# Kernel tuning notes

Hardware: AMD Instinct MI355X
Metric: run time of the kernel (lower is better)

Reference implementation:

```python
import jax, jax.numpy as jnp
import numpy as np

IMAGE_TOKEN = 32000
PAD_TOKEN = 0
IGNORE_INDEX = -100
PATCH = 14
B, S = 8, 1024
IMG = 336
VOCAB = 32064
D = 4096          # text embed_dim
DV = 1024         # vision hidden
N_LAYERS, N_EXPERTS, N_SHARED = 32, 8, 2
NP = (IMG // PATCH) ** 2          # 576 patches after dropping CLS
MAXE = (NP - 1) + S               # one <image> token per row -> 1599


def setup_inputs() -> dict:
    key = jax.random.key(0)
    ks = jax.random.split(key, 12)
    input_ids = jax.random.randint(ks[0], (B, S), 1, IMAGE_TOKEN)  # avoid pad(0) and image token
    input_ids = input_ids.at[:, 5].set(IMAGE_TOKEN)                # exactly one image token per row
    pixel_values = jax.random.normal(ks[1], (B, 3, IMG, IMG), jnp.float32)
    attention_mask = jnp.ones((B, S), jnp.int32)
    labels = jax.random.randint(ks[2], (B, S), 0, IMAGE_TOKEN)
    embed_table = jax.random.normal(ks[3], (VOCAB, D), jnp.float32) * 0.02
    cls_emb = jax.random.normal(ks[4], (DV,), jnp.float32) * 0.02
    patch_w = jax.random.normal(ks[5], (3 * PATCH * PATCH, DV), jnp.float32) * 0.02
    patch_b = jax.random.normal(ks[6], (DV,), jnp.float32) * 0.02
    proj_w1 = jax.random.normal(ks[7], (DV, D), jnp.float32) * 0.02
    proj_b1 = jax.random.normal(ks[8], (D,), jnp.float32) * 0.02
    proj_w2 = jax.random.normal(ks[9], (D, D), jnp.float32) * 0.02
    proj_b2 = jax.random.normal(ks[10], (D,), jnp.float32) * 0.02
    return dict(input_ids=input_ids, pixel_values=pixel_values, attention_mask=attention_mask,
                labels=labels, embed_table=embed_table, cls_emb=cls_emb, patch_w=patch_w,
                patch_b=patch_b, proj_w1=proj_w1, proj_b1=proj_b1, proj_w2=proj_w2, proj_b2=proj_b2)


def _vision_project(pixel_values, cls_emb, patch_w, patch_b, w1, b1, w2, b2):
    # Vision tower stub: patchify + linear patch embedding, CLS prepended,
    # then 'default' select strategy drops CLS, then 2-layer GELU projector.
    n = pixel_values.shape[0]
    g = IMG // PATCH
    x = pixel_values.reshape(n, 3, g, PATCH, g, PATCH)
    x = x.transpose(0, 2, 4, 1, 3, 5).reshape(n, g * g, 3 * PATCH * PATCH)
    h = x @ patch_w + patch_b                                   # [n, 576, DV]
    hidden = jnp.concatenate([jnp.broadcast_to(cls_emb, (n, 1, DV)), h], axis=1)  # [n, 577, DV]
    sel = hidden[:, 1:]                                          # drop CLS ('default')
    return jax.nn.gelu(sel @ w1 + b1) @ w2 + b2                  # [n, 576, D]


def _merge(image_features, inputs_embeds, input_ids, attention_mask, labels):
    b, s = input_ids.shape
    n, p, d = image_features.shape
    special = input_ids == IMAGE_TOKEN                           # [B,S]
    left_padding = jnp.sum(input_ids[:, -1] == PAD_TOKEN) == 0
    new_pos = jnp.cumsum(special.astype(jnp.int32) * (p - 1) + 1, axis=-1) - 1
    nb_pad = MAXE - 1 - new_pos[:, -1]
    new_pos = new_pos + jnp.where(left_padding, nb_pad[:, None], 0)
    pos_safe = jnp.where(special, MAXE, new_pos)                 # OOB index for image tokens -> dropped
    bi = jnp.arange(b)[:, None]
    final_emb = jnp.zeros((b, MAXE, d), inputs_embeds.dtype).at[bi, pos_safe].set(inputs_embeds, mode='drop')
    final_attn = jnp.zeros((b, MAXE), attention_mask.dtype).at[bi, pos_safe].set(attention_mask, mode='drop')
    final_labels = jnp.full((b, MAXE), IGNORE_INDEX, labels.dtype).at[bi, pos_safe].set(labels, mode='drop')
    img_ow = jnp.all(final_emb == 0, axis=-1)                    # slots never written by text
    img_ow = img_ow & (jnp.cumsum(img_ow.astype(jnp.int32), axis=-1) - 1 >= nb_pad[:, None])
    flat_mask = img_ow.reshape(-1)                               # [B*MAXE]
    rank = jnp.cumsum(flat_mask.astype(jnp.int32)) - 1           # row-major rank of each True slot
    img_flat = image_features.reshape(-1, d)                     # [n*p, D]
    gathered = img_flat[jnp.clip(rank, 0, img_flat.shape[0] - 1)]
    final_emb = jnp.where(flat_mask[:, None], gathered, final_emb.reshape(-1, d)).reshape(b, MAXE, d)
    final_attn = jnp.where(img_ow, jnp.ones_like(final_attn), final_attn)
    return final_emb, final_attn, final_labels


def reference(input_ids, pixel_values, attention_mask, labels, embed_table, cls_emb,
              patch_w, patch_b, proj_w1, proj_b1, proj_w2, proj_b2):
    inputs_embeds = embed_table[input_ids]                       # [B,S,D]
    image_features = _vision_project(pixel_values, cls_emb, patch_w, patch_b,
                                     proj_w1, proj_b1, proj_w2, proj_b2)
    final_emb, final_attn, final_labels = _merge(image_features, inputs_embeds,
                                                 input_ids, attention_mask, labels)
    # torch.empty buffers (uninitialized scratch) -> zeros for determinism
    router_logits = jnp.zeros((N_LAYERS, MAXE, N_EXPERTS), jnp.float32)
    shared_router_logits = jnp.zeros((N_LAYERS, MAXE, N_SHARED), jnp.float32)
    current_layer = jnp.int32(0)
    return (current_layer, final_emb, final_attn, final_labels, router_logits, shared_router_logits)
```

## Files before the change

kernel.cpp:

```cpp
#include <hip/hip_runtime.h>
#include <math.h>

#define B_ 8
#define S_ 1024
#define D_ 4096
#define DV_ 1024
#define NP_ 576
#define MAXE_ 1599
#define PK_ 588
#define IMG_ 336
#define GRID_ 24
#define PATCH_ 14
#define IMAGE_TOKEN_ 32000
#define PAD_TOKEN_ 0
#define NLAYERS_ 32
#define NEXP_ 8
#define NSH_ 2

#define EMB_ELEMS ((size_t)B_ * MAXE_ * D_)
#define OFF_EMB   ((size_t)1)
#define OFF_ATTN  (OFF_EMB + EMB_ELEMS)
#define OFF_LAB   (OFF_ATTN + (size_t)B_ * MAXE_)
#define OFF_ROUTER (OFF_LAB + (size_t)B_ * MAXE_)
#define ROUTER_ELEMS ((size_t)NLAYERS_ * MAXE_ * (NEXP_ + NSH_))

typedef __bf16 bf16x8 __attribute__((ext_vector_type(8)));
typedef float  f32x4  __attribute__((ext_vector_type(4)));
typedef unsigned short ushort_t;

__device__ __forceinline__ unsigned short f2bf(float f) {
    unsigned u = __float_as_uint(f);
    u += 0x7fffu + ((u >> 16) & 1u);
    return (unsigned short)(u >> 16);
}

__device__ __forceinline__ void async_copy16(const void* g, void* l) {
    __builtin_amdgcn_global_load_lds(
        (const __attribute__((address_space(1))) void*)g,
        (__attribute__((address_space(3))) void*)l, 16, 0, 0);
}

__global__ void fill_tail_kernel(float* __restrict__ out) {
    size_t i = (size_t)blockIdx.x * blockDim.x + threadIdx.x;
    if (i == 0) out[0] = 0.0f;
    for (size_t j = i; j < ROUTER_ELEMS; j += (size_t)gridDim.x * blockDim.x)
        out[OFF_ROUTER + j] = 0.0f;
}

__global__ __launch_bounds__(512) void merge_kernel(
    const int* __restrict__ input_ids, const int* __restrict__ attn_mask,
    const int* __restrict__ labels, float* __restrict__ out,
    int* __restrict__ src_index, int* __restrict__ img_pos)
{
    __shared__ int sh_nbpad[B_];
    __shared__ int sh_shift[B_];
    __shared__ int sh_nqual[B_];
    __shared__ int sh_leftpad;
    float* out_attn = out + OFF_ATTN;
    float* out_lab  = out + OFF_LAB;
    const int tid = threadIdx.x;

    for (int i = tid; i < B_ * MAXE_; i += blockDim.x) {
        src_index[i] = -1;
        out_attn[i] = 0.0f;
        out_lab[i] = -100.0f;
    }
    for (int i = tid; i < B_ * NP_; i += blockDim.x) img_pos[i] = -1;
    if (tid == 0) {
        int anypad = 0;
        for (int b = 0; b < B_; b++)
            if (input_ids[b * S_ + S_ - 1] == PAD_TOKEN_) anypad = 1;
        sh_leftpad = !anypad;
    }
    __syncthreads();

    const int wave = tid >> 6;
    const int lane = tid & 63;
    const unsigned long long below = (1ull << lane) - 1ull;

    if (wave < B_) {
        const int b = wave;
        int nspec = 0;
        for (int c = 0; c < S_; c += 64) {
            int id = input_ids[b * S_ + c + lane];
            nspec += __popcll(__ballot(id == IMAGE_TOKEN_));
        }
        int nb_pad = MAXE_ - S_ - (NP_ - 1) * nspec;
        int shift = sh_leftpad ? nb_pad : 0;
        int nholes = MAXE_ - (S_ - nspec);
        int nq = nholes - nb_pad; if (nq < 0) nq = 0;
        if (lane == 0) { sh_nbpad[b] = nb_pad; sh_shift[b] = shift; sh_nqual[b] = nq; }
        int carry = 0;
        for (int c = 0; c < S_; c += 64) {
            int t = c + lane;
            int id = input_ids[b * S_ + t];
            int spec = (id == IMAGE_TOKEN_);
            unsigned long long m = __ballot(spec);
            int nbefore = carry + __popcll(m & below);
            if (!spec) {
                int pos = t + (NP_ - 1) * nbefore + shift;
                if (pos >= 0 && pos < MAXE_) {
                    src_index[b * MAXE_ + pos] = t;
                    out_attn[b * MAXE_ + pos] = (float)attn_mask[b * S_ + t];
                    out_lab[b * MAXE_ + pos]  = (float)labels[b * S_ + t];
                }
            }
            carry += __popcll(m);
        }
    }
    __syncthreads();

    if (wave < B_) {
        const int b = wave;
        int offs = 0;
        for (int r = 0; r < b; r++) offs += sh_nqual[r];
        const int nb_pad = sh_nbpad[b];
        int hcarry = 0;
        for (int c = 0; c < MAXE_; c += 64) {
            int p = c + lane;
            int flag = 0;
            if (p < MAXE_) flag = (src_index[b * MAXE_ + p] == -1);
            unsigned long long m = __ballot(flag);
            int h = hcarry + __popcll(m & below);
            if (flag && h >= nb_pad) {
                int g = offs + (h - nb_pad);
                if (g > B_ * NP_ - 1) g = B_ * NP_ - 1;
                if (g < 0) g = 0;
                img_pos[g] = b * MAXE_ + p;
                src_index[b * MAXE_ + p] = -2;
                out_attn[b * MAXE_ + p] = 1.0f;
            }
            hcarry += __popcll(m);
        }
    }
}

__global__ void patchify_kernel(const float* __restrict__ pix, float* __restrict__ x) {
    int i = blockIdx.x * blockDim.x + threadIdx.x;
    const int total = B_ * NP_ * PK_;
    if (i >= total) return;
    int q = i % PK_;
    int t = (i / PK_) % NP_;
    int n = i / (PK_ * NP_);
    int c = q / (PATCH_ * PATCH_);
    int r = q % (PATCH_ * PATCH_);
    int py = r / PATCH_, px = r % PATCH_;
    int gy = t / GRID_, gx = t % GRID_;
    x[i] = pix[(((size_t)n * 3 + c) * IMG_ + gy * PATCH_ + py) * IMG_ + gx * PATCH_ + px];
}

__global__ __launch_bounds__(256) void transpose_bf16_kernel(
    const float* __restrict__ src, ushort_t* __restrict__ dst, int R, int C)
{
    __shared__ float tile[32][33];
    int c0 = blockIdx.x * 32, r0 = blockIdx.y * 32;
    int tx = threadIdx.x & 31, ty = threadIdx.x >> 5;
    for (int i = ty; i < 32; i += 8)
        tile[i][tx] = src[(size_t)(r0 + i) * C + c0 + tx];
    __syncthreads();
    for (int i = ty; i < 32; i += 8)
        dst[(size_t)(c0 + i) * R + r0 + tx] = f2bf(tile[tx][i]);
}

__global__ __launch_bounds__(256) void sgemm_kernel(
    const float* __restrict__ A, const float* __restrict__ Bm,
    const float* __restrict__ bias, float* __restrict__ C, ushort_t* __restrict__ Cb,
    int M, int N, int K, int mode)
{
    __shared__ float As[8][128 + 4];
    __shared__ float Bs[8][128 + 4];
    const int tid = threadIdx.x;
    const int tx = tid & 15;
    const int ty = tid >> 4;
    const int row0 = blockIdx.y * 128;
    const int col0 = blockIdx.x * 128;
    float acc[8][8];
#pragma unroll
    for (int i = 0; i < 8; i++)
#pragma unroll
        for (int j = 0; j < 8; j++) acc[i][j] = 0.0f;

    const int ar = tid >> 1;
    const int ak = (tid & 1) * 4;
    const int bk = tid >> 5;
    const int bn = (tid & 31) * 4;

    for (int k0 = 0; k0 < K; k0 += 8) {
        float4 av = make_float4(0.f, 0.f, 0.f, 0.f);
        {
            int r = row0 + ar;
            int kb = k0 + ak;
            if (r < M) {
                if (kb + 4 <= K) {
                    av = *(const float4*)(A + (size_t)r * K + kb);
                } else {
                    float tmp[4] = {0.f, 0.f, 0.f, 0.f};
                    for (int u = 0; u < 4; u++)
                        if (kb + u < K) tmp[u] = A[(size_t)r * K + kb + u];
                    av = make_float4(tmp[0], tmp[1], tmp[2], tmp[3]);
                }
            }
        }
        As[ak + 0][ar] = av.x; As[ak + 1][ar] = av.y;
        As[ak + 2][ar] = av.z; As[ak + 3][ar] = av.w;

        float4 bv = make_float4(0.f, 0.f, 0.f, 0.f);
        {
            int kr = k0 + bk;
            if (kr < K) bv = *(const float4*)(Bm + (size_t)kr * N + col0 + bn);
        }
        *(float4*)&Bs[bk][bn] = bv;
        __syncthreads();

#pragma unroll
        for (int kk = 0; kk < 8; kk++) {
            float am[8], bb[8];
#pragma unroll
            for (int i = 0; i < 8; i++) am[i] = As[kk][ty * 8 + i];
#pragma unroll
            for (int j = 0; j < 8; j++) bb[j] = Bs[kk][tx * 8 + j];
#pragma unroll
            for (int i = 0; i < 8; i++)
#pragma unroll
                for (int j = 0; j < 8; j++)
                    acc[i][j] = fmaf(am[i], bb[j], acc[i][j]);
        }
        __syncthreads();
    }

#pragma unroll
    for (int i = 0; i < 8; i++) {
        int r = row0 + ty * 8 + i;
        if (r >= M) continue;
        int c0 = col0 + tx * 8;
        float v[8];
#pragma unroll
        for (int j = 0; j < 8; j++) v[j] = acc[i][j] + bias[c0 + j];
        if (mode == 3) {
            ushort_t* dst = Cb + (size_t)r * N + c0;
#pragma unroll
            for (int j = 0; j < 8; j++) dst[j] = f2bf(v[j]);
        } else {
            float* dst = C + (size_t)r * N + c0;
            *(float4*)dst = make_float4(v[0], v[1], v[2], v[3]);
            *(float4*)(dst + 4) = make_float4(v[4], v[5], v[6], v[7]);
        }
    }
}

__global__ __launch_bounds__(256) void mfma_gemm_bt(
    const ushort_t* __restrict__ A, const ushort_t* __restrict__ Bt,
    const float* __restrict__ bias, ushort_t* __restrict__ outb,
    float* __restrict__ outf, const int* __restrict__ pos_map,
    int M, int N, int K, int mode)
{
    __shared__ ushort_t As[128 * 32];
    __shared__ ushort_t Bs[128 * 32];
    const int tid  = threadIdx.x;
    const int wave = tid >> 6;
    const int lane = tid & 63;
    const int l16  = lane & 15;
    const int quad = lane >> 4;
    const int wrow = (wave >> 1) * 64;
    const int wcol = (wave & 1) * 64;
    const int row0 = blockIdx.y * 128;
    const int col0 = blockIdx.x * 128;

    f32x4 acc[4][4];
#pragma unroll
    for (int i = 0; i < 4; i++)
#pragma unroll
        for (int j = 0; j < 4; j++) acc[i][j] = (f32x4)(0.0f);

    const int R0a = wave * 32;
    const int lr  = lane >> 2;
    const int lc  = (lane & 3) * 8;

    for (int k0 = 0; k0 < K; k0 += 32) {
#pragma unroll
        for (int i = 0; i < 2; i++) {
            int R0 = R0a + i * 16;
            const ushort_t* ga = A  + (size_t)(row0 + R0 + lr) * K + k0 + lc;
            const ushort_t* gb = Bt + (size_t)(col0 + R0 + lr) * K + k0 + lc;
            async_copy16(ga, &As[R0 * 32]);
            async_copy16(gb, &Bs[R0 * 32]);
        }
        __syncthreads();

        bf16x8 af[4], bf[4];
#pragma unroll
        for (int mt = 0; mt < 4; mt++)
            af[mt] = *(const bf16x8*)&As[(wrow + mt * 16 + l16) * 32 + quad * 8];
#pragma unroll
        for (int nt = 0; nt < 4; nt++)
            bf[nt] = *(const bf16x8*)&Bs[(wcol + nt * 16 + l16) * 32 + quad * 8];
#pragma unroll
        for (int mt = 0; mt < 4; mt++)
#pragma unroll
            for (int nt = 0; nt < 4; nt++)
                acc[mt][nt] = __builtin_amdgcn_mfma_f32_16x16x32_bf16(
                    af[mt], bf[nt], acc[mt][nt], 0, 0, 0);
        __syncthreads();
    }

    float bv[4];
#pragma unroll
    for (int nt = 0; nt < 4; nt++) bv[nt] = bias[col0 + wcol + nt * 16 + l16];

#pragma unroll
    for (int mt = 0; mt < 4; mt++) {
#pragma unroll
        for (int r = 0; r < 4; r++) {
            int row = row0 + wrow + mt * 16 + quad * 4 + r;
            if (mode == 2) {
                int orow = pos_map[row];
                if (orow < 0) continue;
#pragma unroll
                for (int nt = 0; nt < 4; nt++) {
                    int col = col0 + wcol + nt * 16 + l16;
                    outf[(size_t)orow * N + col] = acc[mt][nt][r] + bv[nt];
                }
            } else {
#pragma unroll
                for (int nt = 0; nt < 4; nt++) {
                    int col = col0 + wcol + nt * 16 + l16;
                    float x = acc[mt][nt][r] + bv[nt];
                    float u = 0.7978845608028654f * (x + 0.044715f * x * x * x);
                    x = 0.5f * x * (1.0f + tanhf(u));
                    outb[(size_t)row * N + col] = f2bf(x);
                }
            }
        }
    }
}

__global__ __launch_bounds__(256) void scatter_text_kernel(
    const int* __restrict__ src_index, const int* __restrict__ input_ids,
    const float* __restrict__ embed, float* __restrict__ final_emb)
{
    int row = blockIdx.x;
    int src = src_index[row];
    if (src == -2) return;
    float* dst = final_emb + (size_t)row * D_;
    if (src >= 0) {
        int b = row / MAXE_;
        int tok = input_ids[b * S_ + src];
        const float* s = embed + (size_t)tok * D_;
        for (int i = threadIdx.x; i < D_; i += blockDim.x) dst[i] = s[i];
    } else {
        for (int i = threadIdx.x; i < D_; i += blockDim.x) dst[i] = 0.0f;
    }
}

extern "C" void kernel_launch(void* const* d_in, const int* in_sizes, int n_in,
                              void* d_out, int out_size, void* d_ws, size_t ws_size,
                              hipStream_t stream)
{
    const int*   input_ids = (const int*)d_in[0];
    const float* pixel     = (const float*)d_in[1];
    const int*   attn      = (const int*)d_in[2];
    const int*   labels    = (const int*)d_in[3];
    const float* embed     = (const float*)d_in[4];
    const float* patch_w   = (const float*)d_in[6];
    const float* patch_b   = (const float*)d_in[7];
    const float* w1        = (const float*)d_in[8];
    const float* b1        = (const float*)d_in[9];
    const float* w2        = (const float*)d_in[10];
    const float* b2        = (const float*)d_in[11];
    float* out = (float*)d_out;

    char* w = (char*)d_ws;
    int* src_index = (int*)w;
    int* img_pos   = (int*)(w + 51200);
    float* xbuf    = (float*)(w + 51200 + 18432);
    ushort_t* hbuf = (ushort_t*)(xbuf + (size_t)B_ * NP_ * PK_);
    ushort_t* g1   = hbuf + (size_t)B_ * NP_ * DV_;
    ushort_t* w1t  = g1 + (size_t)B_ * NP_ * D_;
    ushort_t* w2t  = w1t + (size_t)D_ * DV_;

    fill_tail_kernel<<<2048, 256, 0, stream>>>(out);
    merge_kernel<<<1, 512, 0, stream>>>(input_ids, attn, labels, out, src_index, img_pos);

    {
        int total = B_ * NP_ * PK_;
        patchify_kernel<<<(total + 255) / 256, 256, 0, stream>>>(pixel, xbuf);
    }
    transpose_bf16_kernel<<<dim3(D_ / 32, DV_ / 32), 256, 0, stream>>>(w1, w1t, DV_, D_);
    transpose_bf16_kernel<<<dim3(D_ / 32, D_ / 32), 256, 0, stream>>>(w2, w2t, D_, D_);

    const int M = B_ * NP_;
    sgemm_kernel<<<dim3(DV_ / 128, (M + 127) / 128), 256, 0, stream>>>(
        xbuf, patch_w, patch_b, nullptr, hbuf, M, DV_, PK_, 3);
    mfma_gemm_bt<<<dim3(D_ / 128, M / 128), 256, 0, stream>>>(
        hbuf, w1t, b1, g1, nullptr, nullptr, M, D_, DV_, 1);
    mfma_gemm_bt<<<dim3(D_ / 128, M / 128), 256, 0, stream>>>(
        g1, w2t, b2, nullptr, out + OFF_EMB, img_pos, M, D_, D_, 2);

    scatter_text_kernel<<<B_ * MAXE_, 256, 0, stream>>>(src_index, input_ids, embed, out + OFF_EMB);
}
```

Before: 1.217 ms.

## Run patch-embedding GEMM on MFMA with split-bf16 operands

Replaces the fp32 SIMT sgemm for the patch embedding with a bf16 MFMA GEMM that splits each operand into high and low bf16 parts and accumulates three products to keep near-fp32 accuracy. Patchify and the patch weight transpose now emit padded (K=608) hi/lo bf16 buffers. The GELU tanh is rewritten in an exp-based form, and the text scatter uses float4 copies. Trade-offs are the extra split and transpose kernels, three times the MFMA work, and bf16-split rounding error.

Measured after the change: 1.087 ms. 10.6% less time.

```diff
diff --git a/kernel.cpp b/kernel.cpp
--- a/kernel.cpp
+++ b/kernel.cpp
@@ -8,6 +8,7 @@
 #define NP_ 576
 #define MAXE_ 1599
 #define PK_ 588
+#define KP_ 608
 #define IMG_ 336
 #define GRID_ 24
 #define PATCH_ 14
@@ -32,6 +33,10 @@
     unsigned u = __float_as_uint(f);
     u += 0x7fffu + ((u >> 16) & 1u);
     return (unsigned short)(u >> 16);
+}
+
+__device__ __forceinline__ float bf2f(unsigned short u) {
+    return __uint_as_float((unsigned)u << 16);
 }
 
 __device__ __forceinline__ void async_copy16(const void* g, void* l) {
@@ -135,18 +140,27 @@
     }
 }
 
-__global__ void patchify_kernel(const float* __restrict__ pix, float* __restrict__ x) {
+__global__ void patchify_split_kernel(const float* __restrict__ pix,
+                                      ushort_t* __restrict__ xh,
+                                      ushort_t* __restrict__ xl)
+{
     int i = blockIdx.x * blockDim.x + threadIdx.x;
-    const int total = B_ * NP_ * PK_;
+    const int total = B_ * NP_ * KP_;
     if (i >= total) return;
-    int q = i % PK_;
-    int t = (i / PK_) % NP_;
-    int n = i / (PK_ * NP_);
-    int c = q / (PATCH_ * PATCH_);
-    int r = q % (PATCH_ * PATCH_);
-    int py = r / PATCH_, px = r % PATCH_;
-    int gy = t / GRID_, gx = t % GRID_;
-    x[i] = pix[(((size_t)n * 3 + c) * IMG_ + gy * PATCH_ + py) * IMG_ + gx * PATCH_ + px];
+    int q = i % KP_;
+    int t = (i / KP_) % NP_;
+    int n = i / (KP_ * NP_);
+    float v = 0.0f;
+    if (q < PK_) {
+        int c = q / (PATCH_ * PATCH_);
+        int r = q % (PATCH_ * PATCH_);
+        int py = r / PATCH_, px = r % PATCH_;
+        int gy = t / GRID_, gx = t % GRID_;
+        v = pix[(((size_t)n * 3 + c) * IMG_ + gy * PATCH_ + py) * IMG_ + gx * PATCH_ + px];
+    }
+    ushort_t h = f2bf(v);
+    xh[i] = h;
+    xl[i] = f2bf(v - bf2f(h));
 }
 
 __global__ __launch_bounds__(256) void transpose_bf16_kernel(
@@ -162,88 +176,112 @@
         dst[(size_t)(c0 + i) * R + r0 + tx] = f2bf(tile[tx][i]);
 }
 
-__global__ __launch_bounds__(256) void sgemm_kernel(
-    const float* __restrict__ A, const float* __restrict__ Bm,
-    const float* __restrict__ bias, float* __restrict__ C, ushort_t* __restrict__ Cb,
-    int M, int N, int K, int mode)
-{
-    __shared__ float As[8][128 + 4];
-    __shared__ float Bs[8][128 + 4];
-    const int tid = threadIdx.x;
-    const int tx = tid & 15;
-    const int ty = tid >> 4;
+__global__ __launch_bounds__(256) void transpose_split_kernel(
+    const float* __restrict__ src, ushort_t* __restrict__ dh,
+    ushort_t* __restrict__ dl, int R, int C, int RP)
+{
+    __shared__ float tile[32][33];
+    int c0 = blockIdx.x * 32, r0 = blockIdx.y * 32;
+    int tx = threadIdx.x & 31, ty = threadIdx.x >> 5;
+    for (int i = ty; i < 32; i += 8) {
+        float v = 0.0f;
+        if (r0 + i < R && c0 + tx < C) v = src[(size_t)(r0 + i) * C + c0 + tx];
+        tile[i][tx] = v;
+    }
+    __syncthreads();
+    for (int i = ty; i < 32; i += 8) {
+        if (c0 + i < C && r0 + tx < RP) {
+            float v = tile[tx][i];
+            ushort_t h = f2bf(v);
+            dh[(size_t)(c0 + i) * RP + r0 + tx] = h;
+            dl[(size_t)(c0 + i) * RP + r0 + tx] = f2bf(v - bf2f(h));
+        }
+    }
+}
+
+__global__ __launch_bounds__(256) void mfma_gemm_split(
+    const ushort_t* __restrict__ Ah, const ushort_t* __restrict__ Al,
+    const ushort_t* __restrict__ Bth, const ushort_t* __restrict__ Btl,
+    const float* __restrict__ bias, ushort_t* __restrict__ outb,
+    int M, int N, int K)
+{
+    __shared__ ushort_t Ash[128 * 32];
+    __shared__ ushort_t Asl[128 * 32];
+    __shared__ ushort_t Bsh[128 * 32];
+    __shared__ ushort_t Bsl[128 * 32];
+    const int tid  = threadIdx.x;
+    const int wave = tid >> 6;
+    const int lane = tid & 63;
+    const int l16  = lane & 15;
+    const int quad = lane >> 4;
+    const int wrow = (wave >> 1) * 64;
+    const int wcol = (wave & 1) * 64;
     const int row0 = blockIdx.y * 128;
     const int col0 = blockIdx.x * 128;
-    float acc[8][8];
-#pragma unroll
-    for (int i = 0; i < 8; i++)
-#pragma unroll
-        for (int j = 0; j < 8; j++) acc[i][j] = 0.0f;
-
-    const int ar = tid >> 1;
-    const int ak = (tid & 1) * 4;
-    const int bk = tid >> 5;
-    const int bn = (tid & 31) * 4;
-
-    for (int k0 = 0; k0 < K; k0 += 8) {
-        float4 av = make_float4(0.f, 0.f, 0.f, 0.f);
-        {
-            int r = row0 + ar;
-            int kb = k0 + ak;
-            if (r < M) {
-                if (kb + 4 <= K) {
-                    av = *(const float4*)(A + (size_t)r * K + kb);
-                } else {
-                    float tmp[4] = {0.f, 0.f, 0.f, 0.f};
-                    for (int u = 0; u < 4; u++)
-                        if (kb + u < K) tmp[u] = A[(size_t)r * K + kb + u];
-                    av = make_float4(tmp[0], tmp[1], tmp[2], tmp[3]);
-                }
+
+    f32x4 acc[4][4];
+#pragma unroll
+    for (int i = 0; i < 4; i++)
+#pragma unroll
+        for (int j = 0; j < 4; j++) acc[i][j] = (f32x4)(0.0f);
+
+    const int R0a = wave * 32;
+    const int lr  = lane >> 2;
+    const int lc  = (lane & 3) * 8;
+
+    for (int k0 = 0; k0 < K; k0 += 32) {
+#pragma unroll
+        for (int i = 0; i < 2; i++) {
+            int R0 = R0a + i * 16;
+            size_t aoff = (size_t)(row0 + R0 + lr) * K + k0 + lc;
+            size_t boff = (size_t)(col0 + R0 + lr) * K + k0 + lc;
+            async_copy16(Ah  + aoff, &Ash[R0 * 32]);
+            async_copy16(Al  + aoff, &Asl[R0 * 32]);
+            async_copy16(Bth + boff, &Bsh[R0 * 32]);
+            async_copy16(Btl + boff, &Bsl[R0 * 32]);
+        }
+        __syncthreads();
+
+        bf16x8 ah[4], al[4], bh[4], bl[4];
+#pragma unroll
+        for (int mt = 0; mt < 4; mt++) {
+            ah[mt] = *(const bf16x8*)&Ash[(wrow + mt * 16 + l16) * 32 + quad * 8];
+            al[mt] = *(const bf16x8*)&Asl[(wrow + mt * 16 + l16) * 32 + quad * 8];
+        }
+#pragma unroll
+        for (int nt = 0; nt < 4; nt++) {
+            bh[nt] = *(const bf16x8*)&Bsh[(wcol + nt * 16 + l16) * 32 + quad * 8];
+            bl[nt] = *(const bf16x8*)&Bsl[(wcol + nt * 16 + l16) * 32 + quad * 8];
+        }
+#pragma unroll
+        for (int mt = 0; mt < 4; mt++)
+#pragma unroll
+            for (int nt = 0; nt < 4; nt++) {
+                acc[mt][nt] = __builtin_amdgcn_mfma_f32_16x16x32_bf16(
+                    ah[mt], bh[nt], acc[mt][nt], 0, 0, 0);
+                acc[mt][nt] = __builtin_amdgcn_mfma_f32_16x16x32_bf16(
+                    ah[mt], bl[nt], acc[mt][nt], 0, 0, 0);
+                acc[mt][nt] = __builtin_amdgcn_mfma_f32_16x16x32_bf16(
+                    al[mt], bh[nt], acc[mt][nt], 0, 0, 0);
             }
-        }
-        As[ak + 0][ar] = av.x; As[ak + 1][ar] = av.y;
-        As[ak + 2][ar] = av.z; As[ak + 3][ar] = av.w;
-
-        float4 bv = make_float4(0.f, 0.f, 0.f, 0.f);
-        {
-            int kr = k0 + bk;
-            if (kr < K) bv = *(const float4*)(Bm + (size_t)kr * N + col0 + bn);
-        }
-        *(float4*)&Bs[bk][bn] = bv;
         __syncthreads();
-
-#pragma unroll
-        for (int kk = 0; kk < 8; kk++) {
-            float am[8], bb[8];
-#pragma unroll
-            for (int i = 0; i < 8; i++) am[i] = As[kk][ty * 8 + i];
-#pragma unroll
-            for (int j = 0; j < 8; j++) bb[j] = Bs[kk][tx * 8 + j];
-#pragma unroll
-            for (int i = 0; i < 8; i++)
-#pragma unroll
-                for (int j = 0; j < 8; j++)
-                    acc[i][j] = fmaf(am[i], bb[j], acc[i][j]);
-        }
-        __syncthreads();
-    }
-
-#pragma unroll
-    for (int i = 0; i < 8; i++) {
-        int r = row0 + ty * 8 + i;
-        if (r >= M) continue;
-        int c0 = col0 + tx * 8;
-        float v[8];
-#pragma unroll
-        for (int j = 0; j < 8; j++) v[j] = acc[i][j] + bias[c0 + j];
-        if (mode == 3) {
-            ushort_t* dst = Cb + (size_t)r * N + c0;
-#pragma unroll
-            for (int j = 0; j < 8; j++) dst[j] = f2bf(v[j]);
-        } else {
-            float* dst = C + (size_t)r * N + c0;
-            *(float4*)dst = make_float4(v[0], v[1], v[2], v[3]);
-            *(float4*)(dst + 4) = make_float4(v[4], v[5], v[6], v[7]);
+    }
+
+    float bv[4];
+#pragma unroll
+    for (int nt = 0; nt < 4; nt++) bv[nt] = bias[col0 + wcol + nt * 16 + l16];
+
+#pragma unroll
+    for (int mt = 0; mt < 4; mt++) {
+#pragma unroll
+        for (int r = 0; r < 4; r++) {
+            int row = row0 + wrow + mt * 16 + quad * 4 + r;
+            ushort_t* dst = outb + (size_t)row * N;
+#pragma unroll
+            for (int nt = 0; nt < 4; nt++) {
+                int col = col0 + wcol + nt * 16 + l16;
+                dst[col] = f2bf(acc[mt][nt][r] + bv[nt]);
+            }
         }
     }
 }
@@ -326,7 +364,7 @@
                     int col = col0 + wcol + nt * 16 + l16;
                     float x = acc[mt][nt][r] + bv[nt];
                     float u = 0.7978845608028654f * (x + 0.044715f * x * x * x);
-                    x = 0.5f * x * (1.0f + tanhf(u));
+                    x = x / (1.0f + __expf(-2.0f * u));
                     outb[(size_t)row * N + col] = f2bf(x);
                 }
             }
@@ -341,14 +379,17 @@
     int row = blockIdx.x;
     int src = src_index[row];
     if (src == -2) return;
-    float* dst = final_emb + (size_t)row * D_;
+    float4* dst = (float4*)(final_emb + (size_t)row * D_);
     if (src >= 0) {
         int b = row / MAXE_;
         int tok = input_ids[b * S_ + src];
-        const float* s = embed + (size_t)tok * D_;
-        for (int i = threadIdx.x; i < D_; i += blockDim.x) dst[i] = s[i];
+        const float4* s = (const float4*)(embed + (size_t)tok * D_);
+#pragma unroll
+        for (int i = threadIdx.x; i < D_ / 4; i += 256) dst[i] = s[i];
     } else {
-        for (int i = threadIdx.x; i < D_; i += blockDim.x) dst[i] = 0.0f;
+#pragma unroll
+        for (int i = threadIdx.x; i < D_ / 4; i += 256)
+            dst[i] = make_float4(0.f, 0.f, 0.f, 0.f);
     }
 }
 
@@ -372,8 +413,11 @@
     char* w = (char*)d_ws;
     int* src_index = (int*)w;
     int* img_pos   = (int*)(w + 51200);
-    float* xbuf    = (float*)(w + 51200 + 18432);
-    ushort_t* hbuf = (ushort_t*)(xbuf + (size_t)B_ * NP_ * PK_);
+    ushort_t* xh   = (ushort_t*)(w + 51200 + 18432);
+    ushort_t* xl   = xh  + (size_t)B_ * NP_ * KP_;
+    ushort_t* pwh  = xl  + (size_t)B_ * NP_ * KP_;
+    ushort_t* pwl  = pwh + (size_t)DV_ * KP_;
+    ushort_t* hbuf = pwl + (size_t)DV_ * KP_;
     ushort_t* g1   = hbuf + (size_t)B_ * NP_ * DV_;
     ushort_t* w1t  = g1 + (size_t)B_ * NP_ * D_;
     ushort_t* w2t  = w1t + (size_t)D_ * DV_;
@@ -382,15 +426,17 @@
     merge_kernel<<<1, 512, 0, stream>>>(input_ids, attn, labels, out, src_index, img_pos);
 
     {
-        int total = B_ * NP_ * PK_;
-        patchify_kernel<<<(total + 255) / 256, 256, 0, stream>>>(pixel, xbuf);
-    }
+        int total = B_ * NP_ * KP_;
+        patchify_split_kernel<<<(total + 255) / 256, 256, 0, stream>>>(pixel, xh, xl);
+    }
+    transpose_split_kernel<<<dim3(DV_ / 32, KP_ / 32), 256, 0, stream>>>(
+        patch_w, pwh, pwl, PK_, DV_, KP_);
     transpose_bf16_kernel<<<dim3(D_ / 32, DV_ / 32), 256, 0, stream>>>(w1, w1t, DV_, D_);
     transpose_bf16_kernel<<<dim3(D_ / 32, D_ / 32), 256, 0, stream>>>(w2, w2t, D_, D_);
 
     const int M = B_ * NP_;
-    sgemm_kernel<<<dim3(DV_ / 128, (M + 127) / 128), 256, 0, stream>>>(
-        xbuf, patch_w, patch_b, nullptr, hbuf, M, DV_, PK_, 3);
+    mfma_gemm_split<<<dim3(DV_ / 128, M / 128), 256, 0, stream>>>(
+        xh, xl, pwh, pwl, patch_b, hbuf, M, DV_, KP_);
     mfma_gemm_bt<<<dim3(D_ / 128, M / 128), 256, 0, stream>>>(
         hbuf, w1t, b1, g1, nullptr, nullptr, M, D_, DV_, 1);
     mfma_gemm_bt<<<dim3(D_ / 128, M / 128), 256, 0, stream>>>(
```
